# Performance work log

Hardware: AMD Instinct MI355X
Metric: run time of the kernel (lower is better)

Reference implementation:

```python
import jax, jax.numpy as jnp
import numpy as np

ALPHA = 0.5
TEMP = 0.1
TEMP2 = 0.05  # hardcoded in nt_xent_loss2
NUM_CLASSES = 10
EPS = 1e-12


def setup_inputs() -> dict:
    key = jax.random.key(0)
    k1, k2, k3 = jax.random.split(key, 3)
    B, D, C = 4096, 256, NUM_CLASSES
    cls_feats = jax.random.normal(k1, (B, D), dtype=jnp.float32)
    predicts = jax.random.normal(k2, (B, C), dtype=jnp.float32)
    targets = jax.random.randint(k3, (B,), 0, C)
    return {"cls_feats": cls_feats, "predicts": predicts, "targets": targets}


def _nt_xent_loss(feats, labels):
    B = feats.shape[0]
    eye = jnp.eye(B, dtype=bool)
    same = labels[:, None] == labels[None, :]
    mask = (same & ~eye).astype(feats.dtype)            # positives, no diagonal
    s = jnp.einsum('bd,cd->bc', feats, feats) / TEMP     # [B,B]
    s = jnp.where(eye, 0.0, s)                           # subtract diag_embed(diag)
    logits = s - jax.lax.stop_gradient(jnp.max(s, axis=1, keepdims=True))
    log_denom = jnp.log(jnp.sum(jnp.exp(logits), axis=1, keepdims=True) + EPS)
    log_prob = logits * mask - log_denom
    mask_sum = jnp.sum(mask, axis=1)
    mask_sum = jnp.where(mask_sum == 0, 1.0, mask_sum)
    pos_logits = jnp.sum(mask * log_prob, axis=1) / mask_sum
    return -jnp.mean(pos_logits)


def _nt_xent_loss2(feats, labels):
    B = feats.shape[0]
    eye = jnp.eye(B, dtype=bool)
    same = labels[:, None] == labels[None, :]
    mask = (same & ~eye).astype(feats.dtype)
    diff = ~same                                         # mask2 / different-label pairs
    S = (feats @ feats.T) / TEMP2                        # [B,B]
    val = jnp.where(diff, S, 0.0)                        # dot * different_label_mask

    # The torch loop body depends only on labels[i] -> compute once per class.
    def per_class(c):
        neg = labels != c                                # negatives of class c
        in_sub = neg[:, None] & neg[None, :]             # submatrix membership
        # row max over columns restricted to the negative set
        maxdot = jnp.max(jnp.where(neg[None, :], val, -jnp.inf), axis=1)  # [B]
        shifted = jnp.where(in_sub, val - maxdot[:, None], -jnp.inf)
        s_c = jnp.sum(jnp.exp(shifted))                  # exp_terms.sum()
        n_c = jnp.sum(jnp.where(in_sub, diff, False).astype(jnp.float32))
        return s_c, n_c

    sums, counts = jax.lax.map(jax.checkpoint(per_class), jnp.arange(NUM_CLASSES))
    x = sums[labels]                                     # [B] negtive_dot_negtive_sum
    negsum = counts[labels]                              # [B]
    all_zero = jnp.all(negsum == 0)
    x = jnp.where(all_zero, x, x / negsum)
    log_prob_row = -jnp.log(x + EPS)                     # constant across each row
    mask_sum = jnp.sum(mask, axis=1)
    mask_sum_safe = jnp.where(mask_sum == 0, 1.0, mask_sum)
    pos_logits = (mask_sum * log_prob_row) / mask_sum_safe
    return -jnp.mean(pos_logits)


def reference(cls_feats, predicts, targets):
    norm = jnp.maximum(jnp.linalg.norm(cls_feats, axis=-1, keepdims=True), EPS)
    feats = cls_feats / norm                             # F.normalize(dim=-1)
    logp = jax.nn.log_softmax(predicts, axis=-1)
    ce = -jnp.mean(jnp.take_along_axis(logp, targets[:, None], axis=1)[:, 0])
    cl = _nt_xent_loss(feats, targets)
    tl = _nt_xent_loss2(feats, targets)
    return (1.0 - ALPHA) * ce + ALPHA * cl + 0.5 * ALPHA * tl
```

## Files before the change

kernel.cpp:

```cpp
#include <hip/hip_runtime.h>
#include <math.h>

#define B 4096
#define D 256
#define NC 10
#define LDW 65

typedef __attribute__((ext_vector_type(8))) short bf16x8;
typedef __attribute__((ext_vector_type(4))) float f32x4;

__device__ __forceinline__ unsigned short f2bf(float x) {
    unsigned int u = __float_as_uint(x);
    u += 0x7FFFu + ((u >> 16) & 1u);
    return (unsigned short)(u >> 16);
}

__global__ void prep_kernel(const float* __restrict__ feats, const float* __restrict__ pred,
                            const int* __restrict__ tg, unsigned short* __restrict__ fN,
                            int* __restrict__ h, float* __restrict__ scal) {
    __shared__ int histL[16];
    const int t = threadIdx.x, w = t >> 6, l = t & 63;
    const int gid = t >> 4, lg = t & 15;
    const int r0 = blockIdx.x * 64;
    if (t < 16) histL[t] = 0;
    __syncthreads();
#pragma unroll
    for (int it = 0; it < 4; it++) {
        int row = r0 + it * 16 + gid;
        float4 v[4];
#pragma unroll
        for (int k = 0; k < 4; k++) v[k] = ((const float4*)feats)[row * 64 + lg * 4 + k];
        float ss = 0.f;
#pragma unroll
        for (int k = 0; k < 4; k++)
            ss += v[k].x * v[k].x + v[k].y * v[k].y + v[k].z * v[k].z + v[k].w * v[k].w;
#pragma unroll
        for (int o = 1; o < 16; o <<= 1) ss += __shfl_xor(ss, o);
        float inv = 1.0f / fmaxf(sqrtf(ss), 1e-12f);
        bf16x8 o0, o1;
#pragma unroll
        for (int k = 0; k < 4; k++) {
            const float* vp = (const float*)&v[k];
            if (k < 2) {
#pragma unroll
                for (int e = 0; e < 4; e++) o0[k * 4 + e] = (short)f2bf(vp[e] * inv);
            } else {
#pragma unroll
                for (int e = 0; e < 4; e++) o1[(k - 2) * 4 + e] = (short)f2bf(vp[e] * inv);
            }
        }
        ((bf16x8*)fN)[row * 32 + lg * 2 + 0] = o0;
        ((bf16x8*)fN)[row * 32 + lg * 2 + 1] = o1;
    }
    if (w == 0) atomicAdd(&histL[tg[r0 + l]], 1);
    if (w == 1) {
        int row = r0 + l;
        const float* p = pred + row * NC;
        float m = p[0];
#pragma unroll
        for (int c = 1; c < NC; c++) m = fmaxf(m, p[c]);
        float s = 0.f;
#pragma unroll
        for (int c = 0; c < NC; c++) s += __expf(p[c] - m);
        float v = m + logf(s) - p[tg[row]];
#pragma unroll
        for (int o = 1; o < 64; o <<= 1) v += __shfl_xor(v, o);
        if (l == 0) atomicAdd(&scal[0], v);
    }
    __syncthreads();
    if (t < NC && histL[t]) atomicAdd(&h[t], histL[t]);
}

__global__ void scatter_kernel(const int* __restrict__ tg, const int* __restrict__ h,
                               int* __restrict__ ccnt, int* __restrict__ labelP,
                               int* __restrict__ origIdx, int* __restrict__ posOf) {
    __shared__ int cb[16];
    __shared__ int wcnt[4][16];
    __shared__ int wabs[4][16];
    const int t = threadIdx.x, w = t >> 6, l = t & 63;
    const int row = blockIdx.x * 256 + t;
    const int c = tg[row];
    if (t == 0) {
        int s = 0;
        for (int cc = 0; cc < NC; cc++) { cb[cc] = s; s += h[cc]; }
    }
    unsigned long long below = (l == 0) ? 0ull : ((~0ull) >> (64 - l));
    int rank = 0;
#pragma unroll
    for (int cc = 0; cc < NC; cc++) {
        unsigned long long m = __ballot(c == cc);
        if (c == cc) rank = __popcll(m & below);
        if (l == 0) wcnt[w][cc] = __popcll(m);
    }
    __syncthreads();
    if (t < NC) {
        int pre[4], s = 0;
#pragma unroll
        for (int ww = 0; ww < 4; ww++) { pre[ww] = s; s += wcnt[ww][t]; }
        int b = cb[t] + atomicAdd(&ccnt[t], s);
#pragma unroll
        for (int ww = 0; ww < 4; ww++) wabs[ww][t] = b + pre[ww];
    }
    __syncthreads();
    int pos = wabs[w][c] + rank;
    labelP[pos] = c;
    origIdx[pos] = row;
    posOf[row] = pos;
}

__launch_bounds__(256)
__global__ void gemm_kernel(const unsigned short* __restrict__ fN,
                            const int* __restrict__ tg, const int* __restrict__ labelP,
                            const int* __restrict__ origIdx, const int* __restrict__ posOf,
                            float* __restrict__ E1, float* __restrict__ P1,
                            float* __restrict__ E2G, int* __restrict__ M2K) {
    __shared__ float scW[4][16 * LDW];
    __shared__ int labS[256];
    __shared__ float E2L[64 * 11];
    __shared__ int M2L[64 * 11];
    __shared__ float E1L[64], P1L[64];

    const int t = threadIdx.x;
    const int w = t >> 6, l = t & 63;
    const int qr = l >> 4, lm = l & 15;
    const int row0 = blockIdx.x * 64;
    const int colB = blockIdx.y * 256;

    labS[t] = labelP[colB + t];
    for (int s = t; s < 64 * 11; s += 256) { E2L[s] = 0.f; M2L[s] = 0; }
    if (t < 64) { E1L[t] = 0.f; P1L[t] = 0.f; }

    int offB[4];
#pragma unroll
    for (int nb = 0; nb < 4; nb++)
        offB[nb] = origIdx[colB + w * 64 + nb * 16 + lm] * D + qr * 8;

    const unsigned short* pa = fN + (row0 + lm) * D + qr * 8;

    f32x4 acc[4][4];
#pragma unroll
    for (int mb = 0; mb < 4; mb++)
#pragma unroll
        for (int nb = 0; nb < 4; nb++) acc[mb][nb] = (f32x4){0.f, 0.f, 0.f, 0.f};

#pragma unroll 2
    for (int ks = 0; ks < 8; ks++) {
        bf16x8 af[4], bfr[4];
#pragma unroll
        for (int mb = 0; mb < 4; mb++) af[mb] = *(const bf16x8*)(pa + mb * 16 * D + ks * 32);
#pragma unroll
        for (int nb = 0; nb < 4; nb++) bfr[nb] = *(const bf16x8*)(fN + offB[nb] + ks * 32);
#pragma unroll
        for (int mb = 0; mb < 4; mb++)
#pragma unroll
            for (int nb = 0; nb < 4; nb++)
                acc[mb][nb] = __builtin_amdgcn_mfma_f32_16x16x32_bf16(af[mb], bfr[nb],
                                                                      acc[mb][nb], 0, 0, 0);
    }
    __syncthreads();

    for (int mb = 0; mb < 4; mb++) {
#pragma unroll
        for (int nb = 0; nb < 4; nb++)
#pragma unroll
            for (int r = 0; r < 4; r++)
                scW[w][(qr * 4 + r) * LDW + nb * 16 + lm] = acc[mb][nb][r];
        __syncthreads();
        const int rowL = mb * 16 + lm;
        const int rowg = row0 + rowL;
        const int li = tg[rowg];
        const int posr = posOf[rowg];
        const float* srow = &scW[w][lm * LDW + qr * 16];
        const int colg0 = colB + w * 64 + qr * 16;
        float e1sum = 0.f, p1sum = 0.f;
        int seg = -1; float segE = 0.f; int segK = 0;
#pragma unroll
        for (int j = 0; j < 16; j++) {
            float g = srow[j];
            int lj = labS[w * 64 + qr * 16 + j];
            bool diag = (colg0 + j == posr);
            bool same = (lj == li);
            float s1 = diag ? 0.f : 10.f * g;
            float e1 = __expf(s1);
            e1sum += e1;
            p1sum += (same && !diag) ? s1 : 0.f;
            if (lj != seg) {
                if (seg >= 0) {
                    if (segE > 0.f) atomicAdd(&E2L[rowL * 11 + seg], segE);
                    if (segK > 0) atomicMax(&M2L[rowL * 11 + seg], segK);
                }
                seg = lj; segE = 0.f; segK = 0;
            }
            if (!same) {
                segE += e1 * e1;
                segK = max(segK, __float_as_int(20.f * g + 64.f));
            }
        }
        if (seg >= 0) {
            if (segE > 0.f) atomicAdd(&E2L[rowL * 11 + seg], segE);
            if (segK > 0) atomicMax(&M2L[rowL * 11 + seg], segK);
        }
        e1sum += __shfl_xor(e1sum, 16); e1sum += __shfl_xor(e1sum, 32);
        p1sum += __shfl_xor(p1sum, 16); p1sum += __shfl_xor(p1sum, 32);
        if (qr == 0) {
            atomicAdd(&E1L[rowL], e1sum);
            atomicAdd(&P1L[rowL], p1sum);
        }
        __syncthreads();
    }

    if (t < 64) {
        atomicAdd(&E1[row0 + t], E1L[t]);
        atomicAdd(&P1[row0 + t], P1L[t]);
    }
    for (int s = t; s < 64 * NC; s += 256) {
        int r = s / NC, c = s - r * NC;
        float e = E2L[r * 11 + c];
        int k = M2L[r * 11 + c];
        if (e > 0.f) atomicAdd(&E2G[(row0 + r) * NC + c], e);
        if (k > 0) atomicMax(&M2K[(row0 + r) * NC + c], k);
    }
}

__global__ void rowfin_kernel(const int* __restrict__ tg, const int* __restrict__ h,
                              const float* __restrict__ E1, const float* __restrict__ P1,
                              const float* __restrict__ E2G, const int* __restrict__ M2K,
                              float* __restrict__ sums, float* __restrict__ scal,
                              int* __restrict__ done, float* __restrict__ out) {
    __shared__ float ssumL[16];
    __shared__ int lastS;
    const int t = threadIdx.x;
    if (t < 16) ssumL[t] = 0.f;
    __syncthreads();
    const int i = blockIdx.x * 64 + t;
    const int li = tg[i];
    float E2[NC], M2[NC];
#pragma unroll
    for (int k = 0; k < NC; k++) {
        E2[k] = E2G[i * NC + k];
        int key = M2K[i * NC + k];
        M2[k] = (key > 0) ? (__int_as_float(key) - 64.f) : -3.0e38f;
    }
    const int hl = h[li];
    E2[li] = (float)hl;
    M2[li] = 0.f;
    float m1 = -3.0e38f, m2 = -3.0e38f;
    int a1 = -1;
#pragma unroll
    for (int k = 0; k < NC; k++) {
        float v = M2[k];
        if (v > m1) { m2 = m1; m1 = v; a1 = k; }
        else if (v > m2) m2 = v;
    }
    float Es = 0.f;
#pragma unroll
    for (int k = 0; k < NC; k++) Es += E2[k];
#pragma unroll
    for (int c = 0; c < NC; c++) {
        if (c == li) continue;
        float T = Es - E2[c];
        if (T > 0.f) {
            float md = (a1 == c) ? m2 : m1;
            atomicAdd(&ssumL[c], __expf(-md) * T);
        }
    }
    float cn = (float)(hl - 1);
    float pos1 = (cn > 0.f) ? (P1[i] / cn - logf(E1[i])) : 0.f;
#pragma unroll
    for (int o = 1; o < 64; o <<= 1) pos1 += __shfl_xor(pos1, o);
    if (t == 0) atomicAdd(&scal[1], pos1);
    __syncthreads();
    if (t < NC && ssumL[t] > 0.f) atomicAdd(&sums[t], ssumL[t]);

    __threadfence();
    if (t == 0) lastS = (atomicAdd(done, 1) == 63);
    __syncthreads();
    if (lastS && t == 0) {
        int hh[NC];
        long long S2 = 0;
        for (int c = 0; c < NC; c++) { hh[c] = h[c]; S2 += (long long)hh[c] * hh[c]; }
        float ncs[NC];
        int az = 1;
        for (int c = 0; c < NC; c++) {
            long long M = (long long)B - hh[c];
            long long n = M * M - (S2 - (long long)hh[c] * hh[c]);
            ncs[c] = (float)n;
            if (hh[c] > 0 && n != 0) az = 0;
        }
        float possum = 0.f;
        for (int c = 0; c < NC; c++) {
            if (hh[c] > 1) {
                float x = atomicAdd(&sums[c], 0.f);
                if (!az) x = x / ncs[c];
                possum += (float)hh[c] * (-logf(x + 1e-12f));
            }
        }
        float ce = scal[0] / (float)B;
        float cl = -(atomicAdd(&scal[1], 0.f) / (float)B);
        float tl = -(possum / (float)B);
        float loss = 0.5f * ce + 0.5f * cl + 0.25f * tl;
        unsigned int bits = __float_as_uint(loss);
        unsigned int hedged = (bits & 0xFFFF0000u) | (bits >> 16);
        *(unsigned int*)out = hedged;
    }
}

extern "C" void kernel_launch(void* const* d_in, const int* in_sizes, int n_in,
                              void* d_out, int out_size, void* d_ws, size_t ws_size,
                              hipStream_t stream) {
    (void)in_sizes; (void)n_in; (void)out_size; (void)ws_size;
    const float* feats = (const float*)d_in[0];
    const float* pred = (const float*)d_in[1];
    const int* tg = (const int*)d_in[2];
    float* out = (float*)d_out;

    unsigned short* fN = (unsigned short*)d_ws;
    float* E1 = (float*)(fN + B * D);
    float* P1 = E1 + B;
    float* E2G = P1 + B;
    int* M2K = (int*)(E2G + B * NC);
    int* h = M2K + B * NC;
    int* ccnt = h + 16;
    float* sums = (float*)(ccnt + 16);
    float* scal = sums + 16;
    int* done = (int*)(scal + 16);
    int* labelP = done + 16;
    int* origIdx = labelP + B;
    int* posOf = origIdx + B;

    size_t zeroBytes = (size_t)((char*)(done + 16) - (char*)E1);
    hipMemsetAsync(E1, 0, zeroBytes, stream);

    prep_kernel<<<B / 64, 256, 0, stream>>>(feats, pred, tg, fN, h, scal);
    scatter_kernel<<<B / 256, 256, 0, stream>>>(tg, h, ccnt, labelP, origIdx, posOf);
    gemm_kernel<<<dim3(B / 64, B / 256), 256, 0, stream>>>(fN, tg, labelP, origIdx, posOf,
                                                           E1, P1, E2G, M2K);
    rowfin_kernel<<<B / 64, 64, 0, stream>>>(tg, h, E1, P1, E2G, M2K, sums, scal, done, out);
}
```

Baseline: 151.7 us.

## Fuse workspace zeroing into prep kernel, widen prep grid, drop per-tile GEMM barriers

The large accumulator-buffer memset moves into prep_kernel, with each thread zeroing one float4, and only a small header region is still cleared by hipMemsetAsync. prep_kernel now handles 16 rows per block instead of 64, giving four times as many blocks. In the GEMM epilogue, row labels and positions are loaded into registers up front, and the per-mb __syncthreads around the per-warp scratch tile are removed. This cuts memset and barrier overhead, but dropping the barriers relies on each warp reading only its own scW slice, with correctness depending on wavefront-level ordering of LDS writes and reads.

```diff
diff --git a/kernel.cpp b/kernel.cpp
--- a/kernel.cpp
+++ b/kernel.cpp
@@ -5,6 +5,7 @@
 #define D 256
 #define NC 10
 #define LDW 65
+#define ZERO4 22528
 
 typedef __attribute__((ext_vector_type(8))) short bf16x8;
 typedef __attribute__((ext_vector_type(4))) float f32x4;
@@ -17,55 +18,56 @@
 
 __global__ void prep_kernel(const float* __restrict__ feats, const float* __restrict__ pred,
                             const int* __restrict__ tg, unsigned short* __restrict__ fN,
-                            int* __restrict__ h, float* __restrict__ scal) {
+                            float4* __restrict__ bigz, int* __restrict__ h,
+                            float* __restrict__ scal) {
     __shared__ int histL[16];
     const int t = threadIdx.x, w = t >> 6, l = t & 63;
     const int gid = t >> 4, lg = t & 15;
-    const int r0 = blockIdx.x * 64;
+    const int r0 = blockIdx.x * 16;
     if (t < 16) histL[t] = 0;
     __syncthreads();
-#pragma unroll
-    for (int it = 0; it < 4; it++) {
-        int row = r0 + it * 16 + gid;
-        float4 v[4];
-#pragma unroll
-        for (int k = 0; k < 4; k++) v[k] = ((const float4*)feats)[row * 64 + lg * 4 + k];
-        float ss = 0.f;
-#pragma unroll
-        for (int k = 0; k < 4; k++)
-            ss += v[k].x * v[k].x + v[k].y * v[k].y + v[k].z * v[k].z + v[k].w * v[k].w;
-#pragma unroll
-        for (int o = 1; o < 16; o <<= 1) ss += __shfl_xor(ss, o);
-        float inv = 1.0f / fmaxf(sqrtf(ss), 1e-12f);
-        bf16x8 o0, o1;
-#pragma unroll
-        for (int k = 0; k < 4; k++) {
-            const float* vp = (const float*)&v[k];
-            if (k < 2) {
-#pragma unroll
-                for (int e = 0; e < 4; e++) o0[k * 4 + e] = (short)f2bf(vp[e] * inv);
-            } else {
-#pragma unroll
-                for (int e = 0; e < 4; e++) o1[(k - 2) * 4 + e] = (short)f2bf(vp[e] * inv);
-            }
-        }
-        ((bf16x8*)fN)[row * 32 + lg * 2 + 0] = o0;
-        ((bf16x8*)fN)[row * 32 + lg * 2 + 1] = o1;
-    }
-    if (w == 0) atomicAdd(&histL[tg[r0 + l]], 1);
-    if (w == 1) {
-        int row = r0 + l;
-        const float* p = pred + row * NC;
+    int zi = blockIdx.x * 256 + t;
+    if (zi < ZERO4) bigz[zi] = (float4){0.f, 0.f, 0.f, 0.f};
+
+    int row = r0 + gid;
+    float4 v[4];
+#pragma unroll
+    for (int k = 0; k < 4; k++) v[k] = ((const float4*)feats)[row * 64 + lg * 4 + k];
+    float ss = 0.f;
+#pragma unroll
+    for (int k = 0; k < 4; k++)
+        ss += v[k].x * v[k].x + v[k].y * v[k].y + v[k].z * v[k].z + v[k].w * v[k].w;
+#pragma unroll
+    for (int o = 1; o < 16; o <<= 1) ss += __shfl_xor(ss, o);
+    float inv = 1.0f / fmaxf(sqrtf(ss), 1e-12f);
+    bf16x8 o0, o1;
+#pragma unroll
+    for (int k = 0; k < 4; k++) {
+        const float* vp = (const float*)&v[k];
+        if (k < 2) {
+#pragma unroll
+            for (int e = 0; e < 4; e++) o0[k * 4 + e] = (short)f2bf(vp[e] * inv);
+        } else {
+#pragma unroll
+            for (int e = 0; e < 4; e++) o1[(k - 2) * 4 + e] = (short)f2bf(vp[e] * inv);
+        }
+    }
+    ((bf16x8*)fN)[row * 32 + lg * 2 + 0] = o0;
+    ((bf16x8*)fN)[row * 32 + lg * 2 + 1] = o1;
+
+    if (w == 0 && l < 16) atomicAdd(&histL[tg[r0 + l]], 1);
+    if (w == 1 && l < 16) {
+        const float* p = pred + (r0 + l) * NC;
         float m = p[0];
 #pragma unroll
         for (int c = 1; c < NC; c++) m = fmaxf(m, p[c]);
         float s = 0.f;
 #pragma unroll
         for (int c = 0; c < NC; c++) s += __expf(p[c] - m);
-        float v = m + logf(s) - p[tg[row]];
-#pragma unroll
-        for (int o = 1; o < 64; o <<= 1) v += __shfl_xor(v, o);
-        if (l == 0) atomicAdd(&scal[0], v);
+        float vce = m + logf(s) - p[tg[r0 + l]];
+#pragma unroll
+        for (int o = 1; o < 16; o <<= 1) vce += __shfl_xor(vce, o);
+        if (l == 0) atomicAdd(&scal[0], vce);
     }
     __syncthreads();
     if (t < NC && histL[t]) atomicAdd(&h[t], histL[t]);
@@ -159,17 +161,24 @@
     }
     __syncthreads();
 
+    int liR[4], posR[4];
+#pragma unroll
+    for (int mb = 0; mb < 4; mb++) {
+        int rg = row0 + mb * 16 + lm;
+        liR[mb] = tg[rg];
+        posR[mb] = posOf[rg];
+    }
+
+#pragma unroll
     for (int mb = 0; mb < 4; mb++) {
 #pragma unroll
         for (int nb = 0; nb < 4; nb++)
 #pragma unroll
             for (int r = 0; r < 4; r++)
                 scW[w][(qr * 4 + r) * LDW + nb * 16 + lm] = acc[mb][nb][r];
-        __syncthreads();
         const int rowL = mb * 16 + lm;
-        const int rowg = row0 + rowL;
-        const int li = tg[rowg];
-        const int posr = posOf[rowg];
+        const int li = liR[mb];
+        const int posr = posR[mb];
         const float* srow = &scW[w][lm * LDW + qr * 16];
         const int colg0 = colB + w * 64 + qr * 16;
         float e1sum = 0.f, p1sum = 0.f;
@@ -206,8 +215,8 @@
             atomicAdd(&E1L[rowL], e1sum);
             atomicAdd(&P1L[rowL], p1sum);
         }
-        __syncthreads();
-    }
+    }
+    __syncthreads();
 
     if (t < 64) {
         atomicAdd(&E1[row0 + t], E1L[t]);
@@ -328,10 +337,9 @@
     int* origIdx = labelP + B;
     int* posOf = origIdx + B;
 
-    size_t zeroBytes = (size_t)((char*)(done + 16) - (char*)E1);
-    hipMemsetAsync(E1, 0, zeroBytes, stream);
-
-    prep_kernel<<<B / 64, 256, 0, stream>>>(feats, pred, tg, fN, h, scal);
+    hipMemsetAsync(h, 0, 5 * 16 * sizeof(int), stream);
+
+    prep_kernel<<<B / 16, 256, 0, stream>>>(feats, pred, tg, fN, (float4*)E1, h, scal);
     scatter_kernel<<<B / 256, 256, 0, stream>>>(tg, h, ccnt, labelP, origIdx, posOf);
     gemm_kernel<<<dim3(B / 64, B / 256), 256, 0, stream>>>(fN, tg, labelP, origIdx, posOf,
                                                            E1, P1, E2G, M2K);
```

Measured after the change: 141.1 us. 7.0% less time.
